# Kernel optimization log

Hardware: AMD Instinct MI355X
Metric: run time of the kernel (lower is better)

The kernel has to match this reference:

```python
import jax, jax.numpy as jnp
import numpy as np

B, S, E, H = 4, 2048, 1280, 5


def setup_inputs() -> dict:
    key = jax.random.key(0)
    ks = jax.random.split(key, 5)
    scale = 1.0 / np.sqrt(E)
    return {
        "x": jax.random.normal(ks[0], (B, S, E), dtype=jnp.float32),
        "Wq": jax.random.normal(ks[1], (E, E), dtype=jnp.float32) * scale,
        "Wk": jax.random.normal(ks[2], (E, E), dtype=jnp.float32) * scale,
        "Wv": jax.random.normal(ks[3], (E, E), dtype=jnp.float32) * scale,
        "Wu": jax.random.normal(ks[4], (E, E), dtype=jnp.float32) * scale,
        "bu": jnp.zeros((E,), dtype=jnp.float32),
    }


def reference(x, Wq, Wk, Wv, Wu, bu):
    b, s_len, e = x.shape
    h = H
    d = e // h
    # torch nn.Linear: y = x @ W.T
    q = (x @ Wq.T).reshape(b, s_len, h, d).transpose(0, 2, 1, 3)  # b h s d
    k = (x @ Wk.T).reshape(b, s_len, h, d).transpose(0, 2, 1, 3)
    v = (x @ Wv.T).reshape(b, s_len, h, d).transpose(0, 2, 1, 3)
    # NOTE: original scales by sqrt(emb_dim), not sqrt(head_dim)
    scores = jnp.einsum("bhqd,bhkd->bhqk", q, k) / (e ** 0.5)
    # 'upper diag matrix' mask: strictly-upper-triangular positions -> -inf (causal)
    causal = jnp.triu(jnp.ones((s_len, s_len), dtype=bool), k=1)
    scores = jnp.where(causal[None, None], jnp.float32(-jnp.inf), scores)
    att = jax.nn.softmax(scores, axis=-1)
    out = jnp.einsum("bhqk,bhkd->bhqd", att, v)
    out = out.transpose(0, 2, 1, 3).reshape(b, s_len, e)
    return out @ Wu.T + bu
```

## Files before the change

### kernel.cpp

```cpp
#include <hip/hip_runtime.h>
#include <hip/hip_bf16.h>
#include <stdint.h>

#define B_  4
#define S_  2048
#define E_  1280
#define H_  5
#define D_  256
#define BH_ 20
#define M_  8192
#define K_  1280

#define SCALE_ 0.027950849718747372f

typedef __attribute__((ext_vector_type(8))) __bf16 bf16x8;
typedef __attribute__((ext_vector_type(4))) float  f32x4;

__device__ __forceinline__ ushort f2bf(float f) {
  union { float f; uint32_t u; } v; v.f = f;
  return (ushort)((v.u + 0x7FFFu + ((v.u >> 16) & 1u)) >> 16);
}

typedef const __attribute__((address_space(1))) void* gas_cvp;
typedef __attribute__((address_space(3))) void*       las_vp;

__device__ __forceinline__ void glds16(const void* g, void* l) {
  __builtin_amdgcn_global_load_lds((gas_cvp)g, (las_vp)l, 16, 0, 0);
}

__global__ void cvt_bf16_kernel(const float4* __restrict__ in,
                                ushort4* __restrict__ out, int n4) {
  int i = blockIdx.x * blockDim.x + threadIdx.x;
  int stride = gridDim.x * blockDim.x;
  for (; i < n4; i += stride) {
    float4 v = in[i];
    ushort4 u;
    u.x = f2bf(v.x); u.y = f2bf(v.y); u.z = f2bf(v.z); u.w = f2bf(v.w);
    out[i] = u;
  }
}

template<int MODE>
__global__ __launch_bounds__(256, 2)
void gemm_bt(const ushort* __restrict__ A, const ushort* __restrict__ W,
             ushort* __restrict__ OB, float* __restrict__ OF,
             const float* __restrict__ bias)
{
  __shared__ __align__(16) ushort Abuf[128 * 64];
  __shared__ __align__(16) ushort Bbuf[128 * 64];
  const int tid  = threadIdx.x;
  const int lane = tid & 63;
  const int wid  = tid >> 6;
  const int m0 = blockIdx.x * 128;
  const int n0 = blockIdx.y * 128;
  const int wr = (wid >> 1) * 64;
  const int wc = (wid & 1) * 64;

  f32x4 acc[4][4] = {};

  const int soff = wid * 4096 + lane * 16;

  for (int kk = 0; kk < K_; kk += 64) {
    __syncthreads();
#pragma unroll
    for (int i = 0; i < 4; ++i) {
      int off = soff + i * 1024;
      int row = off >> 7;
      int c8  = (off >> 4) & 7;
      int s8  = c8 ^ (row & 7);
      glds16(A + (size_t)(m0 + row) * K_ + kk + s8 * 8,
             (char*)Abuf + wid * 4096 + i * 1024);
      glds16(W + (size_t)(n0 + row) * K_ + kk + s8 * 8,
             (char*)Bbuf + wid * 4096 + i * 1024);
    }
    __syncthreads();
#pragma unroll
    for (int kt = 0; kt < 2; ++kt) {
      bf16x8 af[4], bfr[4];
#pragma unroll
      for (int mf = 0; mf < 4; ++mf) {
        int row  = wr + mf * 16 + (lane & 15);
        int byte = (row << 7) + kt * 64 + ((lane >> 4) << 4);
        af[mf] = *(const bf16x8*)((const char*)Abuf + (byte ^ ((row & 7) << 4)));
      }
#pragma unroll
      for (int nf = 0; nf < 4; ++nf) {
        int row  = wc + nf * 16 + (lane & 15);
        int byte = (row << 7) + kt * 64 + ((lane >> 4) << 4);
        bfr[nf] = *(const bf16x8*)((const char*)Bbuf + (byte ^ ((row & 7) << 4)));
      }
#pragma unroll
      for (int mf = 0; mf < 4; ++mf)
#pragma unroll
        for (int nf = 0; nf < 4; ++nf)
          acc[mf][nf] = __builtin_amdgcn_mfma_f32_16x16x32_bf16(
              af[mf], bfr[nf], acc[mf][nf], 0, 0, 0);
    }
  }

#pragma unroll
  for (int mf = 0; mf < 4; ++mf) {
#pragma unroll
    for (int nf = 0; nf < 4; ++nf) {
      int mbase = m0 + wr + mf * 16 + ((lane >> 4) << 2);
      int n     = n0 + wc + nf * 16 + (lane & 15);
      if (MODE == 2) {
        float bv = bias[n];
#pragma unroll
        for (int r = 0; r < 4; ++r) {
          int m = mbase + r;
          OF[(size_t)m * E_ + n] = acc[mf][nf][r] + bv;
        }
      } else if (MODE == 0) {
        int h = n >> 8, dd = n & 255;
#pragma unroll
        for (int r = 0; r < 4; ++r) {
          int m = mbase + r;
          int b = m >> 11, s = m & 2047;
          OB[((size_t)((b * H_ + h) * S_ + s)) * D_ + dd] = f2bf(acc[mf][nf][r]);
        }
      } else {
        int h = n >> 8, dd = n & 255;
        size_t idx = ((size_t)((mbase >> 11) * H_ + h) * D_ + dd) * S_ + (mbase & 2047);
        ushort4 pk;
        pk.x = f2bf(acc[mf][nf][0]);
        pk.y = f2bf(acc[mf][nf][1]);
        pk.z = f2bf(acc[mf][nf][2]);
        pk.w = f2bf(acc[mf][nf][3]);
        *(ushort4*)(OB + idx) = pk;
      }
    }
  }
}

__global__ __launch_bounds__(256, 2)
void flash_attn_kernel(const ushort* __restrict__ Q, const ushort* __restrict__ Kg,
                       const ushort* __restrict__ Vt, ushort* __restrict__ AO)
{
  __shared__ __align__(16) ushort Kbuf[2][32 * 256];
  __shared__ __align__(16) ushort Vbuf[2][256 * 32];
  __shared__ __align__(16) char   Pbuf[4 * 16 * 80];

  const int tid  = threadIdx.x;
  const int lane = tid & 63;
  const int wid  = tid >> 6;
  const int l15  = lane & 15;
  const int l4   = lane >> 4;

  const int id  = blockIdx.x;
  const int idp = (id & 7) * 80 + (id >> 3);
  const int bh  = idp >> 5;
  const int tq  = 31 - (idp & 31);
  const int bq0 = tq * 64;
  const int q0w = bq0 + wid * 16;

  const ushort* Qb = Q  + (size_t)bh * S_ * D_;
  const ushort* Kb = Kg + (size_t)bh * S_ * D_;
  const ushort* Vb = Vt + (size_t)bh * D_ * S_;

  bf16x8 aq[8];
  {
    const ushort* qrow = Qb + (size_t)(q0w + l15) * D_ + l4 * 8;
#pragma unroll
    for (int kt = 0; kt < 8; ++kt) aq[kt] = *(const bf16x8*)(qrow + kt * 32);
  }

  f32x4 o[16] = {};
  float m_r[4], l_r[4];
#pragma unroll
  for (int r = 0; r < 4; ++r) { m_r[r] = -1e30f; l_r[r] = 0.f; }

  char* Pw = Pbuf + wid * 1280;
  const int nt = 2 * tq + 2;

#define STAGE_KV(bufi, kvbase)                                                \
  do {                                                                        \
    _Pragma("unroll")                                                         \
    for (int i_ = 0; i_ < 4; ++i_) {                                          \
      int off_ = wid * 4096 + i_ * 1024 + lane * 16;                          \
      int rK_  = off_ >> 9;                                                   \
      int s8_  = ((off_ >> 4) & 31) ^ (rK_ & 7);                              \
      glds16(Kb + (size_t)((kvbase) + rK_) * D_ + s8_ * 8,                    \
             (char*)Kbuf[bufi] + wid * 4096 + i_ * 1024);                     \
      int rV_  = off_ >> 6;                                                   \
      glds16(Vb + (size_t)rV_ * S_ + (kvbase) + ((off_ & 63) >> 1),           \
             (char*)Vbuf[bufi] + wid * 4096 + i_ * 1024);                     \
    }                                                                         \
  } while (0)

  STAGE_KV(0, 0);
  __syncthreads();

  int cur = 0;
  for (int t = 0; t < nt; ++t) {
    const int kv0 = t * 32;
    if (t + 1 < nt) STAGE_KV(cur ^ 1, kv0 + 32);

    if (kv0 <= q0w + 15) {
      f32x4 sacc[2] = {};
      const char* kb = (const char*)Kbuf[cur];
      __builtin_amdgcn_s_setprio(1);
#pragma unroll
      for (int kt = 0; kt < 8; ++kt) {
#pragma unroll
        for (int h2 = 0; h2 < 2; ++h2) {
          int n    = h2 * 16 + l15;
          int byte = (n << 9) + kt * 64 + (l4 << 4);
          bf16x8 bk = *(const bf16x8*)(kb + (byte ^ ((n & 7) << 4)));
          sacc[h2] = __builtin_amdgcn_mfma_f32_16x16x32_bf16(aq[kt], bk, sacc[h2], 0, 0, 0);
        }
      }
      __builtin_amdgcn_s_setprio(0);

      const bool msk = (kv0 + 31 > q0w);
      float sv[2][4];
#pragma unroll
      for (int h2 = 0; h2 < 2; ++h2) {
        int kvc = kv0 + h2 * 16 + l15;
#pragma unroll
        for (int r = 0; r < 4; ++r) {
          float s = sacc[h2][r] * SCALE_;
          if (msk && kvc > q0w + l4 * 4 + r) s = -1e30f;
          sv[h2][r] = s;
        }
      }
      float pm[4];
#pragma unroll
      for (int r = 0; r < 4; ++r) pm[r] = fmaxf(sv[0][r], sv[1][r]);
#pragma unroll
      for (int d = 1; d < 16; d <<= 1)
#pragma unroll
        for (int r = 0; r < 4; ++r)
          pm[r] = fmaxf(pm[r], __shfl_xor(pm[r], d, 64));

      bool grow = false;
#pragma unroll
      for (int r = 0; r < 4; ++r) grow = grow || (pm[r] > m_r[r] + 8.f);
      float rs[4];
      if (__any(grow)) {
        float alpha[4];
#pragma unroll
        for (int r = 0; r < 4; ++r) {
          float mn = fmaxf(m_r[r], pm[r]);
          alpha[r] = __expf(m_r[r] - mn);
          m_r[r]   = mn;
        }
#pragma unroll
        for (int h2 = 0; h2 < 2; ++h2)
#pragma unroll
          for (int r = 0; r < 4; ++r)
            sv[h2][r] = __expf(sv[h2][r] - m_r[r]);
#pragma unroll
        for (int r = 0; r < 4; ++r) rs[r] = sv[0][r] + sv[1][r];
#pragma unroll
        for (int d = 1; d < 16; d <<= 1)
#pragma unroll
          for (int r = 0; r < 4; ++r)
            rs[r] += __shfl_xor(rs[r], d, 64);
#pragma unroll
        for (int r = 0; r < 4; ++r) l_r[r] = l_r[r] * alpha[r] + rs[r];
#pragma unroll
        for (int nf = 0; nf < 16; ++nf)
#pragma unroll
          for (int r = 0; r < 4; ++r) o[nf][r] *= alpha[r];
      } else {
#pragma unroll
        for (int h2 = 0; h2 < 2; ++h2)
#pragma unroll
          for (int r = 0; r < 4; ++r)
            sv[h2][r] = __expf(sv[h2][r] - m_r[r]);
#pragma unroll
        for (int r = 0; r < 4; ++r) rs[r] = sv[0][r] + sv[1][r];
#pragma unroll
        for (int d = 1; d < 16; d <<= 1)
#pragma unroll
          for (int r = 0; r < 4; ++r)
            rs[r] += __shfl_xor(rs[r], d, 64);
#pragma unroll
        for (int r = 0; r < 4; ++r) l_r[r] += rs[r];
      }

#pragma unroll
      for (int h2 = 0; h2 < 2; ++h2)
#pragma unroll
        for (int r = 0; r < 4; ++r)
          *(ushort*)(Pw + (l4 * 4 + r) * 80 + (h2 * 16 + l15) * 2) = f2bf(sv[h2][r]);
      bf16x8 pa = *(const bf16x8*)(Pw + l15 * 80 + l4 * 16);

      const char* vb = (const char*)Vbuf[cur];
      __builtin_amdgcn_s_setprio(1);
#pragma unroll
      for (int nf = 0; nf < 16; ++nf) {
        bf16x8 bv = *(const bf16x8*)(vb + ((nf * 16 + l15) << 6) + (l4 << 4));
        o[nf] = __builtin_amdgcn_mfma_f32_16x16x32_bf16(pa, bv, o[nf], 0, 0, 0);
      }
      __builtin_amdgcn_s_setprio(0);
    }

    __syncthreads();
    cur ^= 1;
  }
#undef STAGE_KV

  float inv[4];
#pragma unroll
  for (int r = 0; r < 4; ++r) inv[r] = 1.0f / l_r[r];
  int b = bh / H_, h = bh % H_;
  const int dd0 = h * D_;
#pragma unroll
  for (int nf = 0; nf < 16; ++nf) {
    int dd = dd0 + nf * 16 + l15;
#pragma unroll
    for (int r = 0; r < 4; ++r) {
      int s = q0w + l4 * 4 + r;
      AO[(size_t)(b * S_ + s) * E_ + dd] = f2bf(o[nf][r] * inv[r]);
    }
  }
}

extern "C" void kernel_launch(void* const* d_in, const int* in_sizes, int n_in,
                              void* d_out, int out_size, void* d_ws, size_t ws_size,
                              hipStream_t stream) {
  const float* x  = (const float*)d_in[0];
  const float* Wq = (const float*)d_in[1];
  const float* Wk = (const float*)d_in[2];
  const float* Wv = (const float*)d_in[3];
  const float* Wu = (const float*)d_in[4];
  const float* bu = (const float*)d_in[5];

  char* ws = (char*)d_ws;
  ushort* xbf = (ushort*)(ws + 0);
  ushort* Wqb = (ushort*)(ws + 20971520);
  ushort* Wkb = (ushort*)(ws + 24248320);
  ushort* Wvb = (ushort*)(ws + 27525120);
  ushort* Wub = (ushort*)(ws + 30801920);
  ushort* Qw  = (ushort*)(ws + 34078720);
  ushort* Kw  = (ushort*)(ws + 55050240);
  ushort* Vtw = (ushort*)(ws + 76021760);
  ushort* AOw = (ushort*)(ws + 96993280);

  cvt_bf16_kernel<<<2048, 256, 0, stream>>>((const float4*)x,  (ushort4*)xbf, M_ * K_ / 4);
  cvt_bf16_kernel<<<800,  256, 0, stream>>>((const float4*)Wq, (ushort4*)Wqb, E_ * E_ / 4);
  cvt_bf16_kernel<<<800,  256, 0, stream>>>((const float4*)Wk, (ushort4*)Wkb, E_ * E_ / 4);
  cvt_bf16_kernel<<<800,  256, 0, stream>>>((const float4*)Wv, (ushort4*)Wvb, E_ * E_ / 4);
  cvt_bf16_kernel<<<800,  256, 0, stream>>>((const float4*)Wu, (ushort4*)Wub, E_ * E_ / 4);

  dim3 gg(M_ / 128, E_ / 128);
  gemm_bt<0><<<gg, 256, 0, stream>>>(xbf, Wqb, Qw,  nullptr, nullptr);
  gemm_bt<0><<<gg, 256, 0, stream>>>(xbf, Wkb, Kw,  nullptr, nullptr);
  gemm_bt<1><<<gg, 256, 0, stream>>>(xbf, Wvb, Vtw, nullptr, nullptr);

  flash_attn_kernel<<<640, 256, 0, stream>>>(Qw, Kw, Vtw, AOw);

  gemm_bt<2><<<gg, 256, 0, stream>>>(AOw, Wub, nullptr, (float*)d_out, bu);
}
```

Baseline: 413.0 us.

## Merge conversion and QKV launches, transpose score MFMA, fold scale into Q

The five fp32-to-bf16 conversions now run as one 2D-grid launch, and the three Q/K/V projection GEMMs run as one launch that picks the weight by blockIdx.y. Attention now computes S^T by swapping the MFMA operands, so each lane owns one query row. That turns the row max/sum reductions into two cross-lane shuffles instead of four per row value, and lets P be written with packed ushort4 stores. The softmax scale is folded into the Q projection epilogue. This cuts launch overhead and softmax shuffle/ALU work, at the cost of extra __shfl calls to remap alpha and 1/l into the output layout, and Q rounded to bf16 after scaling.

```diff
diff --git a/kernel.cpp b/kernel.cpp
--- a/kernel.cpp
+++ b/kernel.cpp
@@ -28,23 +28,122 @@
   __builtin_amdgcn_global_load_lds((gas_cvp)g, (las_vp)l, 16, 0, 0);
 }
 
-__global__ void cvt_bf16_kernel(const float4* __restrict__ in,
-                                ushort4* __restrict__ out, int n4) {
+__global__ void cvt5_kernel(const float4* __restrict__ s0, const float4* __restrict__ s1,
+                            const float4* __restrict__ s2, const float4* __restrict__ s3,
+                            const float4* __restrict__ s4,
+                            ushort4* __restrict__ d0, ushort4* __restrict__ d1,
+                            ushort4* __restrict__ d2, ushort4* __restrict__ d3,
+                            ushort4* __restrict__ d4, int nx, int nw) {
+  int seg = blockIdx.y;
+  const float4* s = (seg == 0) ? s0 : (seg == 1) ? s1 : (seg == 2) ? s2 : (seg == 3) ? s3 : s4;
+  ushort4*       d = (seg == 0) ? d0 : (seg == 1) ? d1 : (seg == 2) ? d2 : (seg == 3) ? d3 : d4;
+  int n4 = (seg == 0) ? nx : nw;
   int i = blockIdx.x * blockDim.x + threadIdx.x;
   int stride = gridDim.x * blockDim.x;
   for (; i < n4; i += stride) {
-    float4 v = in[i];
+    float4 v = s[i];
     ushort4 u;
     u.x = f2bf(v.x); u.y = f2bf(v.y); u.z = f2bf(v.z); u.w = f2bf(v.w);
-    out[i] = u;
-  }
-}
-
-template<int MODE>
+    d[i] = u;
+  }
+}
+
 __global__ __launch_bounds__(256, 2)
-void gemm_bt(const ushort* __restrict__ A, const ushort* __restrict__ W,
-             ushort* __restrict__ OB, float* __restrict__ OF,
-             const float* __restrict__ bias)
+void gemm_qkv(const ushort* __restrict__ A,
+              const ushort* __restrict__ Wq, const ushort* __restrict__ Wk,
+              const ushort* __restrict__ Wv,
+              ushort* __restrict__ Qo, ushort* __restrict__ Ko, ushort* __restrict__ Vo)
+{
+  __shared__ __align__(16) ushort Abuf[128 * 64];
+  __shared__ __align__(16) ushort Bbuf[128 * 64];
+  const int tid  = threadIdx.x;
+  const int lane = tid & 63;
+  const int wid  = tid >> 6;
+  const int m0 = blockIdx.x * 128;
+  const int which = blockIdx.y / 10;
+  const int n0 = (blockIdx.y % 10) * 128;
+  const ushort* W = (which == 0) ? Wq : (which == 1) ? Wk : Wv;
+  const int wr = (wid >> 1) * 64;
+  const int wc = (wid & 1) * 64;
+
+  f32x4 acc[4][4] = {};
+  const int soff = wid * 4096 + lane * 16;
+
+  for (int kk = 0; kk < K_; kk += 64) {
+    __syncthreads();
+#pragma unroll
+    for (int i = 0; i < 4; ++i) {
+      int off = soff + i * 1024;
+      int row = off >> 7;
+      int c8  = (off >> 4) & 7;
+      int s8  = c8 ^ (row & 7);
+      glds16(A + (size_t)(m0 + row) * K_ + kk + s8 * 8,
+             (char*)Abuf + wid * 4096 + i * 1024);
+      glds16(W + (size_t)(n0 + row) * K_ + kk + s8 * 8,
+             (char*)Bbuf + wid * 4096 + i * 1024);
+    }
+    __syncthreads();
+#pragma unroll
+    for (int kt = 0; kt < 2; ++kt) {
+      bf16x8 af[4], bfr[4];
+#pragma unroll
+      for (int mf = 0; mf < 4; ++mf) {
+        int row  = wr + mf * 16 + (lane & 15);
+        int byte = (row << 7) + kt * 64 + ((lane >> 4) << 4);
+        af[mf] = *(const bf16x8*)((const char*)Abuf + (byte ^ ((row & 7) << 4)));
+      }
+#pragma unroll
+      for (int nf = 0; nf < 4; ++nf) {
+        int row  = wc + nf * 16 + (lane & 15);
+        int byte = (row << 7) + kt * 64 + ((lane >> 4) << 4);
+        bfr[nf] = *(const bf16x8*)((const char*)Bbuf + (byte ^ ((row & 7) << 4)));
+      }
+#pragma unroll
+      for (int mf = 0; mf < 4; ++mf)
+#pragma unroll
+        for (int nf = 0; nf < 4; ++nf)
+          acc[mf][nf] = __builtin_amdgcn_mfma_f32_16x16x32_bf16(
+              af[mf], bfr[nf], acc[mf][nf], 0, 0, 0);
+    }
+  }
+
+#pragma unroll
+  for (int mf = 0; mf < 4; ++mf) {
+#pragma unroll
+    for (int nf = 0; nf < 4; ++nf) {
+      int mbase = m0 + wr + mf * 16 + ((lane >> 4) << 2);
+      int n     = n0 + wc + nf * 16 + (lane & 15);
+      int h = n >> 8, dd = n & 255;
+      if (which == 0) {
+#pragma unroll
+        for (int r = 0; r < 4; ++r) {
+          int m = mbase + r;
+          Qo[((size_t)(((m >> 11) * H_ + h) * S_ + (m & 2047))) * D_ + dd] =
+              f2bf(acc[mf][nf][r] * SCALE_);
+        }
+      } else if (which == 1) {
+#pragma unroll
+        for (int r = 0; r < 4; ++r) {
+          int m = mbase + r;
+          Ko[((size_t)(((m >> 11) * H_ + h) * S_ + (m & 2047))) * D_ + dd] =
+              f2bf(acc[mf][nf][r]);
+        }
+      } else {
+        size_t idx = ((size_t)((mbase >> 11) * H_ + h) * D_ + dd) * S_ + (mbase & 2047);
+        ushort4 pk;
+        pk.x = f2bf(acc[mf][nf][0]);
+        pk.y = f2bf(acc[mf][nf][1]);
+        pk.z = f2bf(acc[mf][nf][2]);
+        pk.w = f2bf(acc[mf][nf][3]);
+        *(ushort4*)(Vo + idx) = pk;
+      }
+    }
+  }
+}
+
+__global__ __launch_bounds__(256, 2)
+void gemm_out(const ushort* __restrict__ A, const ushort* __restrict__ W,
+              float* __restrict__ OF, const float* __restrict__ bias)
 {
   __shared__ __align__(16) ushort Abuf[128 * 64];
   __shared__ __align__(16) ushort Bbuf[128 * 64];
@@ -57,7 +156,6 @@
   const int wc = (wid & 1) * 64;
 
   f32x4 acc[4][4] = {};
-
   const int soff = wid * 4096 + lane * 16;
 
   for (int kk = 0; kk < K_; kk += 64) {
@@ -104,31 +202,10 @@
     for (int nf = 0; nf < 4; ++nf) {
       int mbase = m0 + wr + mf * 16 + ((lane >> 4) << 2);
       int n     = n0 + wc + nf * 16 + (lane & 15);
-      if (MODE == 2) {
-        float bv = bias[n];
-#pragma unroll
-        for (int r = 0; r < 4; ++r) {
-          int m = mbase + r;
-          OF[(size_t)m * E_ + n] = acc[mf][nf][r] + bv;
-        }
-      } else if (MODE == 0) {
-        int h = n >> 8, dd = n & 255;
-#pragma unroll
-        for (int r = 0; r < 4; ++r) {
-          int m = mbase + r;
-          int b = m >> 11, s = m & 2047;
-          OB[((size_t)((b * H_ + h) * S_ + s)) * D_ + dd] = f2bf(acc[mf][nf][r]);
-        }
-      } else {
-        int h = n >> 8, dd = n & 255;
-        size_t idx = ((size_t)((mbase >> 11) * H_ + h) * D_ + dd) * S_ + (mbase & 2047);
-        ushort4 pk;
-        pk.x = f2bf(acc[mf][nf][0]);
-        pk.y = f2bf(acc[mf][nf][1]);
-        pk.z = f2bf(acc[mf][nf][2]);
-        pk.w = f2bf(acc[mf][nf][3]);
-        *(ushort4*)(OB + idx) = pk;
-      }
+      float bv = bias[n];
+#pragma unroll
+      for (int r = 0; r < 4; ++r)
+        OF[(size_t)(mbase + r) * E_ + n] = acc[mf][nf][r] + bv;
     }
   }
 }
@@ -141,9 +218,8 @@
   __shared__ __align__(16) ushort Vbuf[2][256 * 32];
   __shared__ __align__(16) char   Pbuf[4 * 16 * 80];
 
-  const int tid  = threadIdx.x;
-  const int lane = tid & 63;
-  const int wid  = tid >> 6;
+  const int lane = threadIdx.x & 63;
+  const int wid  = threadIdx.x >> 6;
   const int l15  = lane & 15;
   const int l4   = lane >> 4;
 
@@ -151,24 +227,21 @@
   const int idp = (id & 7) * 80 + (id >> 3);
   const int bh  = idp >> 5;
   const int tq  = 31 - (idp & 31);
-  const int bq0 = tq * 64;
-  const int q0w = bq0 + wid * 16;
+  const int q0w = tq * 64 + wid * 16;
 
   const ushort* Qb = Q  + (size_t)bh * S_ * D_;
   const ushort* Kb = Kg + (size_t)bh * S_ * D_;
   const ushort* Vb = Vt + (size_t)bh * D_ * S_;
 
-  bf16x8 aq[8];
+  bf16x8 bq[8];
   {
     const ushort* qrow = Qb + (size_t)(q0w + l15) * D_ + l4 * 8;
 #pragma unroll
-    for (int kt = 0; kt < 8; ++kt) aq[kt] = *(const bf16x8*)(qrow + kt * 32);
+    for (int kt = 0; kt < 8; ++kt) bq[kt] = *(const bf16x8*)(qrow + kt * 32);
   }
 
   f32x4 o[16] = {};
-  float m_r[4], l_r[4];
-#pragma unroll
-  for (int r = 0; r < 4; ++r) { m_r[r] = -1e30f; l_r[r] = 0.f; }
+  float m_s = -1e30f, l_s = 0.f;
 
   char* Pw = Pbuf + wid * 1280;
   const int nt = 2 * tq + 2;
@@ -204,10 +277,10 @@
       for (int kt = 0; kt < 8; ++kt) {
 #pragma unroll
         for (int h2 = 0; h2 < 2; ++h2) {
-          int n    = h2 * 16 + l15;
-          int byte = (n << 9) + kt * 64 + (l4 << 4);
-          bf16x8 bk = *(const bf16x8*)(kb + (byte ^ ((n & 7) << 4)));
-          sacc[h2] = __builtin_amdgcn_mfma_f32_16x16x32_bf16(aq[kt], bk, sacc[h2], 0, 0, 0);
+          int row  = h2 * 16 + l15;
+          int byte = (row << 9) + kt * 64 + (l4 << 4);
+          bf16x8 kf = *(const bf16x8*)(kb + (byte ^ ((row & 7) << 4)));
+          sacc[h2] = __builtin_amdgcn_mfma_f32_16x16x32_bf16(kf, bq[kt], sacc[h2], 0, 0, 0);
         }
       }
       __builtin_amdgcn_s_setprio(0);
@@ -215,76 +288,65 @@
       const bool msk = (kv0 + 31 > q0w);
       float sv[2][4];
 #pragma unroll
-      for (int h2 = 0; h2 < 2; ++h2) {
-        int kvc = kv0 + h2 * 16 + l15;
+      for (int h2 = 0; h2 < 2; ++h2)
 #pragma unroll
         for (int r = 0; r < 4; ++r) {
-          float s = sacc[h2][r] * SCALE_;
-          if (msk && kvc > q0w + l4 * 4 + r) s = -1e30f;
+          float s = sacc[h2][r];
+          if (msk && (kv0 + h2 * 16 + l4 * 4 + r > q0w + l15)) s = -1e30f;
           sv[h2][r] = s;
         }
-      }
-      float pm[4];
-#pragma unroll
-      for (int r = 0; r < 4; ++r) pm[r] = fmaxf(sv[0][r], sv[1][r]);
-#pragma unroll
-      for (int d = 1; d < 16; d <<= 1)
+      float pm = sv[0][0];
+#pragma unroll
+      for (int h2 = 0; h2 < 2; ++h2)
+#pragma unroll
+        for (int r = 0; r < 4; ++r) pm = fmaxf(pm, sv[h2][r]);
+      pm = fmaxf(pm, __shfl_xor(pm, 16, 64));
+      pm = fmaxf(pm, __shfl_xor(pm, 32, 64));
+
+      if (__any(pm > m_s + 8.f)) {
+        float mn = fmaxf(m_s, pm);
+        float alpha = __expf(m_s - mn);
+        m_s = mn;
+#pragma unroll
+        for (int h2 = 0; h2 < 2; ++h2)
+#pragma unroll
+          for (int r = 0; r < 4; ++r) sv[h2][r] = __expf(sv[h2][r] - m_s);
+        float rs = 0.f;
+#pragma unroll
+        for (int h2 = 0; h2 < 2; ++h2)
+#pragma unroll
+          for (int r = 0; r < 4; ++r) rs += sv[h2][r];
+        rs += __shfl_xor(rs, 16, 64);
+        rs += __shfl_xor(rs, 32, 64);
+        l_s = l_s * alpha + rs;
+        float al[4];
 #pragma unroll
         for (int r = 0; r < 4; ++r)
-          pm[r] = fmaxf(pm[r], __shfl_xor(pm[r], d, 64));
-
-      bool grow = false;
-#pragma unroll
-      for (int r = 0; r < 4; ++r) grow = grow || (pm[r] > m_r[r] + 8.f);
-      float rs[4];
-      if (__any(grow)) {
-        float alpha[4];
-#pragma unroll
-        for (int r = 0; r < 4; ++r) {
-          float mn = fmaxf(m_r[r], pm[r]);
-          alpha[r] = __expf(m_r[r] - mn);
-          m_r[r]   = mn;
-        }
+          al[r] = __shfl(alpha, (lane & 48) + ((lane & 48) >> 2) + r, 64);
+#pragma unroll
+        for (int nf = 0; nf < 16; ++nf)
+#pragma unroll
+          for (int r = 0; r < 4; ++r) o[nf][r] *= al[r];
+      } else {
 #pragma unroll
         for (int h2 = 0; h2 < 2; ++h2)
 #pragma unroll
-          for (int r = 0; r < 4; ++r)
-            sv[h2][r] = __expf(sv[h2][r] - m_r[r]);
-#pragma unroll
-        for (int r = 0; r < 4; ++r) rs[r] = sv[0][r] + sv[1][r];
-#pragma unroll
-        for (int d = 1; d < 16; d <<= 1)
-#pragma unroll
-          for (int r = 0; r < 4; ++r)
-            rs[r] += __shfl_xor(rs[r], d, 64);
-#pragma unroll
-        for (int r = 0; r < 4; ++r) l_r[r] = l_r[r] * alpha[r] + rs[r];
-#pragma unroll
-        for (int nf = 0; nf < 16; ++nf)
-#pragma unroll
-          for (int r = 0; r < 4; ++r) o[nf][r] *= alpha[r];
-      } else {
+          for (int r = 0; r < 4; ++r) sv[h2][r] = __expf(sv[h2][r] - m_s);
+        float rs = 0.f;
 #pragma unroll
         for (int h2 = 0; h2 < 2; ++h2)
 #pragma unroll
-          for (int r = 0; r < 4; ++r)
-            sv[h2][r] = __expf(sv[h2][r] - m_r[r]);
-#pragma unroll
-        for (int r = 0; r < 4; ++r) rs[r] = sv[0][r] + sv[1][r];
-#pragma unroll
-        for (int d = 1; d < 16; d <<= 1)
-#pragma unroll
-          for (int r = 0; r < 4; ++r)
-            rs[r] += __shfl_xor(rs[r], d, 64);
-#pragma unroll
-        for (int r = 0; r < 4; ++r) l_r[r] += rs[r];
-      }
-
-#pragma unroll
-      for (int h2 = 0; h2 < 2; ++h2)
-#pragma unroll
-        for (int r = 0; r < 4; ++r)
-          *(ushort*)(Pw + (l4 * 4 + r) * 80 + (h2 * 16 + l15) * 2) = f2bf(sv[h2][r]);
+          for (int r = 0; r < 4; ++r) rs += sv[h2][r];
+        rs += __shfl_xor(rs, 16, 64);
+        rs += __shfl_xor(rs, 32, 64);
+        l_s += rs;
+      }
+
+      ushort4 w0, w1;
+      w0.x = f2bf(sv[0][0]); w0.y = f2bf(sv[0][1]); w0.z = f2bf(sv[0][2]); w0.w = f2bf(sv[0][3]);
+      w1.x = f2bf(sv[1][0]); w1.y = f2bf(sv[1][1]); w1.z = f2bf(sv[1][2]); w1.w = f2bf(sv[1][3]);
+      *(ushort4*)(Pw + l15 * 80 + l4 * 8)      = w0;
+      *(ushort4*)(Pw + l15 * 80 + 32 + l4 * 8) = w1;
       bf16x8 pa = *(const bf16x8*)(Pw + l15 * 80 + l4 * 16);
 
       const char* vb = (const char*)Vbuf[cur];
@@ -302,9 +364,11 @@
   }
 #undef STAGE_KV
 
+  float linv = 1.0f / l_s;
   float inv[4];
 #pragma unroll
-  for (int r = 0; r < 4; ++r) inv[r] = 1.0f / l_r[r];
+  for (int r = 0; r < 4; ++r)
+    inv[r] = __shfl(linv, (lane & 48) + ((lane & 48) >> 2) + r, 64);
   int b = bh / H_, h = bh % H_;
   const int dd0 = h * D_;
 #pragma unroll
@@ -339,18 +403,15 @@
   ushort* Vtw = (ushort*)(ws + 76021760);
   ushort* AOw = (ushort*)(ws + 96993280);
 
-  cvt_bf16_kernel<<<2048, 256, 0, stream>>>((const float4*)x,  (ushort4*)xbf, M_ * K_ / 4);
-  cvt_bf16_kernel<<<800,  256, 0, stream>>>((const float4*)Wq, (ushort4*)Wqb, E_ * E_ / 4);
-  cvt_bf16_kernel<<<800,  256, 0, stream>>>((const float4*)Wk, (ushort4*)Wkb, E_ * E_ / 4);
-  cvt_bf16_kernel<<<800,  256, 0, stream>>>((const float4*)Wv, (ushort4*)Wvb, E_ * E_ / 4);
-  cvt_bf16_kernel<<<800,  256, 0, stream>>>((const float4*)Wu, (ushort4*)Wub, E_ * E_ / 4);
-
-  dim3 gg(M_ / 128, E_ / 128);
-  gemm_bt<0><<<gg, 256, 0, stream>>>(xbf, Wqb, Qw,  nullptr, nullptr);
-  gemm_bt<0><<<gg, 256, 0, stream>>>(xbf, Wkb, Kw,  nullptr, nullptr);
-  gemm_bt<1><<<gg, 256, 0, stream>>>(xbf, Wvb, Vtw, nullptr, nullptr);
+  cvt5_kernel<<<dim3(1024, 5), 256, 0, stream>>>(
+      (const float4*)x, (const float4*)Wq, (const float4*)Wk,
+      (const float4*)Wv, (const float4*)Wu,
+      (ushort4*)xbf, (ushort4*)Wqb, (ushort4*)Wkb, (ushort4*)Wvb, (ushort4*)Wub,
+      M_ * K_ / 4, E_ * E_ / 4);
+
+  gemm_qkv<<<dim3(M_ / 128, 30), 256, 0, stream>>>(xbf, Wqb, Wkb, Wvb, Qw, Kw, Vtw);
 
   flash_attn_kernel<<<640, 256, 0, stream>>>(Qw, Kw, Vtw, AOw);
 
-  gemm_bt<2><<<gg, 256, 0, stream>>>(AOw, Wub, nullptr, (float*)d_out, bu);
-}
+  gemm_out<<<dim3(M_ / 128, E_ / 128), 256, 0, stream>>>(AOw, Wub, (float*)d_out, bu);
+}
```

Measured after the change: 387.6 us. -6.2%, faster.
